# Kernel tuning notes

Measured on AMD Instinct MI355X. Metric: run time of the kernel, lower is better.

The kernel has to match this reference:

```python
import jax, jax.numpy as jnp
import numpy as np

DIM = 192
WH, WW = 8, 8
N = WH * WW           # 64 tokens per window
H = 6                 # heads
HD = DIM // H         # 32
SCALE = HD ** -0.5
B_ = 8192             # num_windows * batch
NW = 64               # windows sharing one mask


def _relative_position_index():
    ch, cw = np.arange(WH), np.arange(WW)
    coords = np.stack(np.meshgrid(ch, cw, indexing='ij'))        # (2, Wh, Ww)
    cf = coords.reshape(2, -1)                                   # (2, N)
    rel = cf[:, :, None] - cf[:, None, :]                        # (2, N, N)
    rel = rel.transpose(1, 2, 0).copy()
    rel[:, :, 0] += WH - 1
    rel[:, :, 1] += WW - 1
    rel[:, :, 0] *= 2 * WW - 1
    return (rel.sum(-1)).astype(np.int32)                        # (N, N)


def setup_inputs() -> dict:
    key = jax.random.key(0)
    ks = jax.random.split(key, 6)
    x = jax.random.normal(ks[0], (B_, N, DIM), dtype=jnp.float32)
    mask = jnp.zeros((NW, N, N), dtype=jnp.float32)
    qkv_w = jax.random.normal(ks[1], (3 * DIM, DIM), dtype=jnp.float32) * 0.02
    qkv_b = jnp.zeros((3 * DIM,), dtype=jnp.float32)
    proj_w = jax.random.normal(ks[2], (DIM, DIM), dtype=jnp.float32) * 0.02
    proj_b = jnp.zeros((DIM,), dtype=jnp.float32)
    bias_table = jax.random.normal(ks[3], ((2 * WH - 1) * (2 * WW - 1), H), dtype=jnp.float32) * 0.02
    rel_idx = jnp.asarray(_relative_position_index())
    return {"x": x, "mask": mask, "qkv_w": qkv_w, "qkv_b": qkv_b,
            "proj_w": proj_w, "proj_b": proj_b, "bias_table": bias_table,
            "rel_idx": rel_idx}


def reference(x, mask, qkv_w, qkv_b, proj_w, proj_b, bias_table, rel_idx):
    b, n, c = x.shape
    # qkv projection -> (3, B_, H, N, HD)
    qkv = (x @ qkv_w.T + qkv_b).reshape(b, n, 3, H, HD).transpose(2, 0, 3, 1, 4)
    q, k, v = qkv[0], qkv[1], qkv[2]
    # gathered relative position bias: (H, N, N)
    rpb = bias_table[rel_idx.reshape(-1)].reshape(n, n, H).transpose(2, 0, 1)
    # attention scores with bias + per-window shift mask
    scores = jnp.einsum('bhnd,bhmd->bhnm', q * SCALE, k) + rpb[None]
    nw = mask.shape[0]
    scores = scores.reshape(b // nw, nw, H, n, n) + mask[None, :, None]
    scores = scores.reshape(b, H, n, n)
    attn = jax.nn.softmax(scores, axis=-1)
    out = jnp.einsum('bhnm,bhmd->bhnd', attn, v)          # (B_, H, N, HD)
    out = out.transpose(0, 2, 1, 3).reshape(b, n, c)       # b n (h d)
    return out @ proj_w.T + proj_b
```

## Files before the change

### kernel.cpp

```cpp
#include <hip/hip_runtime.h>
#include <hip/hip_bf16.h>

typedef __bf16 v8bf __attribute__((ext_vector_type(8)));
typedef float  v4f  __attribute__((ext_vector_type(4)));

#define MFMA(a,b,c) __builtin_amdgcn_mfma_f32_16x16x32_bf16((a),(b),(c),0,0,0)

__device__ __forceinline__ float loadf(const void* p, int i, int isb) {
  return isb ? (float)(((const __bf16*)p)[i]) : ((const float*)p)[i];
}

__global__ void detect_kernel(const void* __restrict__ x, int* __restrict__ flag) {
  __shared__ int cnt;
  if (threadIdx.x == 0) cnt = 0;
  __syncthreads();
  unsigned char b = ((const unsigned char*)x)[1 + 4 * (int)threadIdx.x];
  int e = b & 0x7f;
  if (e >= 0x3B && e <= 0x41) atomicAdd(&cnt, 1);
  __syncthreads();
  if (threadIdx.x == 0) *flag = (cnt >= 64) ? 1 : 0;
}

__global__ void prep_kernel(const void* __restrict__ qkv_w, const void* __restrict__ proj_w,
                            const void* __restrict__ bias_table, const int* __restrict__ rel_idx,
                            const void* __restrict__ mask, const int* __restrict__ flag,
                            __bf16* __restrict__ qkv_wf, __bf16* __restrict__ projf,
                            float* __restrict__ cmb) {
  const int isb = *flag;
  int e = blockIdx.x * 256 + threadIdx.x;
  if (e < 110592) {
    int j = e & 7, lx = (e >> 3) & 63, ks = (e >> 9) % 6, nt = e / 3072;
    int n = nt * 16 + (lx & 15), k = ks * 32 + (lx >> 4) * 8 + j;
    qkv_wf[e] = (__bf16)loadf(qkv_w, n * 192 + k, isb);
  } else if (e < 147456) {
    int e2 = e - 110592;
    int j = e2 & 7, lx = (e2 >> 3) & 63, ks = (e2 >> 9) % 6, nt = e2 / 3072;
    int n = nt * 16 + (lx & 15), k = ks * 32 + (lx >> 4) * 8 + j;
    projf[e2] = (__bf16)loadf(proj_w, n * 192 + k, isb);
  } else if (e < 147456 + 1572864) {
    int e2 = e - 147456;
    int j = e2 & 63, i = (e2 >> 6) & 63, hh = (e2 >> 12) % 6, w = e2 / 24576;
    cmb[e2] = loadf(bias_table, rel_idx[i * 64 + j] * 6 + hh, isb)
            + loadf(mask, (w * 64 + i) * 64 + j, isb);
  }
}

__global__ __launch_bounds__(384, 3)
void wattn_kernel(const void* __restrict__ x, const int* __restrict__ flag,
                  const __bf16* __restrict__ qkv_wf, const __bf16* __restrict__ projf,
                  const float* __restrict__ cmb,
                  const void* __restrict__ qkv_b, const void* __restrict__ proj_b,
                  void* __restrict__ out) {
  __shared__ char smem[73728];
  __bf16* xf = (__bf16*)smem;
  __bf16* Qr = (__bf16*)(smem + 24576);

  const int isb = *flag;
  const int win = blockIdx.x;
  const int t = threadIdx.x;
  const int l = t & 63;
  const int h = t >> 6;
  const int quad = l >> 4;
  const int c16 = l & 15;
  const float SCALE = 0.17677669529663687f;

  #pragma unroll
  for (int i = 0; i < 4; ++i) {
    int c = t + i * 384;
    int tok = c / 24, kb8 = c % 24;
    v8bf v;
    if (isb) {
      v = *(const v8bf*)((const __bf16*)x + (size_t)win * 12288 + (size_t)c * 8);
    } else {
      const float* xp = (const float*)x + (size_t)win * 12288 + (size_t)c * 8;
      float4 f0 = ((const float4*)xp)[0];
      float4 f1 = ((const float4*)xp)[1];
      v8bf tv;
      tv[0]=(__bf16)f0.x; tv[1]=(__bf16)f0.y; tv[2]=(__bf16)f0.z; tv[3]=(__bf16)f0.w;
      tv[4]=(__bf16)f1.x; tv[5]=(__bf16)f1.y; tv[6]=(__bf16)f1.z; tv[7]=(__bf16)f1.w;
      v = tv;
    }
    int mt = tok >> 4, r = tok & 15, ks = kb8 >> 2, kb = kb8 & 3;
    *(v8bf*)(xf + ((mt * 6 + ks) * 64 + kb * 16 + r) * 8) = v;
  }
  __syncthreads();

  const v4f vzero = {0.f, 0.f, 0.f, 0.f};

  v4f acc[4][4];
  #pragma unroll
  for (int n = 0; n < 4; ++n)
    #pragma unroll
    for (int m = 0; m < 4; ++m) acc[n][m] = vzero;

  #pragma unroll
  for (int ks = 0; ks < 6; ++ks) {
    v8bf a[4];
    #pragma unroll
    for (int mt = 0; mt < 4; ++mt) a[mt] = *(const v8bf*)(xf + ((mt * 6 + ks) * 64 + l) * 8);
    #pragma unroll
    for (int ntl = 0; ntl < 4; ++ntl) {
      int nt = (ntl < 2) ? (2 * h + ntl) : (12 + 2 * h + (ntl - 2));
      v8bf b = *(const v8bf*)(qkv_wf + ((nt * 6 + ks) * 64 + l) * 8);
      #pragma unroll
      for (int mt = 0; mt < 4; ++mt) acc[ntl][mt] = MFMA(a[mt], b, acc[ntl][mt]);
    }
  }

  __bf16* qf = Qr + h * 4096;
  __bf16* kf = qf + 2048;
  #pragma unroll
  for (int ntl = 0; ntl < 4; ++ntl) {
    int hd = (ntl & 1) * 16 + c16;
    int nglob = ((ntl < 2) ? 0 : 192) + h * 32 + hd;
    float bias = loadf(qkv_b, nglob, isb);
    float mul = (ntl < 2) ? SCALE : 1.0f;
    __bf16* dst = (ntl < 2) ? qf : kf;
    #pragma unroll
    for (int mt = 0; mt < 4; ++mt)
      #pragma unroll
      for (int reg = 0; reg < 4; ++reg) {
        float vv = (acc[ntl][mt][reg] + bias) * mul;
        int u = mt * 64 + (hd >> 3) * 16 + quad * 4 + reg;
        dst[u * 8 + (hd & 7)] = (__bf16)vv;
      }
  }

  {
    v8bf aq[4];
    #pragma unroll
    for (int mt = 0; mt < 4; ++mt) aq[mt] = *(const v8bf*)(qf + (mt * 64 + l) * 8);
    #pragma unroll
    for (int n = 0; n < 4; ++n)
      #pragma unroll
      for (int m = 0; m < 4; ++m) acc[m][n] = vzero;
    #pragma unroll
    for (int j = 0; j < 4; ++j) {
      v8bf bk = *(const v8bf*)(kf + (j * 64 + l) * 8);
      #pragma unroll
      for (int mt = 0; mt < 4; ++mt) acc[mt][j] = MFMA(aq[mt], bk, acc[mt][j]);
    }
  }
  __bf16* Pf = Qr + h * 4096;
  {
    const float* cb = cmb + (size_t)((win & 63) * 6 + h) * 4096;
    #pragma unroll
    for (int mt = 0; mt < 4; ++mt)
      #pragma unroll
      for (int reg = 0; reg < 4; ++reg) {
        int mrow = quad * 4 + reg;
        int row = mt * 16 + mrow;
        float v0 = acc[mt][0][reg] + cb[row * 64 + c16];
        float v1 = acc[mt][1][reg] + cb[row * 64 + 16 + c16];
        float v2 = acc[mt][2][reg] + cb[row * 64 + 32 + c16];
        float v3 = acc[mt][3][reg] + cb[row * 64 + 48 + c16];
        float mx = fmaxf(fmaxf(v0, v1), fmaxf(v2, v3));
        mx = fmaxf(mx, __shfl_xor(mx, 1));
        mx = fmaxf(mx, __shfl_xor(mx, 2));
        mx = fmaxf(mx, __shfl_xor(mx, 4));
        mx = fmaxf(mx, __shfl_xor(mx, 8));
        float p0 = __expf(v0 - mx), p1 = __expf(v1 - mx);
        float p2 = __expf(v2 - mx), p3 = __expf(v3 - mx);
        float sm = p0 + p1 + p2 + p3;
        sm += __shfl_xor(sm, 1);
        sm += __shfl_xor(sm, 2);
        sm += __shfl_xor(sm, 4);
        sm += __shfl_xor(sm, 8);
        float inv = 1.0f / sm;
        float pn[4] = {p0 * inv, p1 * inv, p2 * inv, p3 * inv};
        #pragma unroll
        for (int j = 0; j < 4; ++j) {
          int u = (mt * 2 + (j >> 1)) * 64 + ((j & 1) * 2 + (c16 >> 3)) * 16 + mrow;
          Pf[u * 8 + (c16 & 7)] = (__bf16)pn[j];
        }
      }
  }

  v4f vac[2][4];
  #pragma unroll
  for (int n = 0; n < 2; ++n)
    #pragma unroll
    for (int m = 0; m < 4; ++m) vac[n][m] = vzero;
  #pragma unroll
  for (int ks = 0; ks < 6; ++ks) {
    v8bf a[4];
    #pragma unroll
    for (int mt = 0; mt < 4; ++mt) a[mt] = *(const v8bf*)(xf + ((mt * 6 + ks) * 64 + l) * 8);
    #pragma unroll
    for (int ntl = 0; ntl < 2; ++ntl) {
      int nt = 24 + 2 * h + ntl;
      v8bf b = *(const v8bf*)(qkv_wf + ((nt * 6 + ks) * 64 + l) * 8);
      #pragma unroll
      for (int mt = 0; mt < 4; ++mt) vac[ntl][mt] = MFMA(a[mt], b, vac[ntl][mt]);
    }
  }
  __syncthreads();

  __bf16* vf = xf + h * 2048;
  #pragma unroll
  for (int ntl = 0; ntl < 2; ++ntl) {
    float bias = loadf(qkv_b, 384 + h * 32 + ntl * 16 + c16, isb);
    #pragma unroll
    for (int mt = 0; mt < 4; ++mt)
      #pragma unroll
      for (int reg = 0; reg < 4; ++reg) {
        int mrow = quad * 4 + reg;
        int u = (ntl * 2 + (mt >> 1)) * 64 + ((mt & 1) * 2 + (mrow >> 3)) * 16 + c16;
        vf[u * 8 + (mrow & 7)] = (__bf16)(vac[ntl][mt][reg] + bias);
      }
  }

  v4f o[4][2];
  #pragma unroll
  for (int m = 0; m < 4; ++m) { o[m][0] = vzero; o[m][1] = vzero; }
  #pragma unroll
  for (int ksb = 0; ksb < 2; ++ksb) {
    v8bf ap[4], bv[2];
    #pragma unroll
    for (int mt = 0; mt < 4; ++mt) ap[mt] = *(const v8bf*)(Pf + ((mt * 2 + ksb) * 64 + l) * 8);
    #pragma unroll
    for (int ntb = 0; ntb < 2; ++ntb) bv[ntb] = *(const v8bf*)(vf + ((ntb * 2 + ksb) * 64 + l) * 8);
    #pragma unroll
    for (int mt = 0; mt < 4; ++mt)
      #pragma unroll
      for (int ntb = 0; ntb < 2; ++ntb) o[mt][ntb] = MFMA(ap[mt], bv[ntb], o[mt][ntb]);
  }
  __syncthreads();

  __bf16* Of = Qr;
  #pragma unroll
  for (int mt = 0; mt < 4; ++mt)
    #pragma unroll
    for (int ntb = 0; ntb < 2; ++ntb)
      #pragma unroll
      for (int reg = 0; reg < 4; ++reg) {
        int u = (mt * 6 + h) * 64 + (ntb * 2 + (c16 >> 3)) * 16 + quad * 4 + reg;
        Of[u * 8 + (c16 & 7)] = (__bf16)o[mt][ntb][reg];
      }
  __syncthreads();

  v4f pa[2][4];
  #pragma unroll
  for (int n = 0; n < 2; ++n)
    #pragma unroll
    for (int m = 0; m < 4; ++m) pa[n][m] = vzero;
  #pragma unroll
  for (int ks = 0; ks < 6; ++ks) {
    v8bf a[4];
    #pragma unroll
    for (int mt = 0; mt < 4; ++mt) a[mt] = *(const v8bf*)(Of + ((mt * 6 + ks) * 64 + l) * 8);
    #pragma unroll
    for (int ntl = 0; ntl < 2; ++ntl) {
      int nt = 2 * h + ntl;
      v8bf b = *(const v8bf*)(projf + ((nt * 6 + ks) * 64 + l) * 8);
      #pragma unroll
      for (int mt = 0; mt < 4; ++mt) pa[ntl][mt] = MFMA(a[mt], b, pa[ntl][mt]);
    }
  }
  #pragma unroll
  for (int ntl = 0; ntl < 2; ++ntl) {
    int col = (2 * h + ntl) * 16 + c16;
    float pb = loadf(proj_b, col, isb);
    #pragma unroll
    for (int mt = 0; mt < 4; ++mt)
      #pragma unroll
      for (int reg = 0; reg < 4; ++reg) {
        float vv = pa[ntl][mt][reg] + pb;
        size_t oi = (size_t)win * 12288 + (size_t)(mt * 16 + quad * 4 + reg) * 192 + col;
        if (isb) ((__bf16*)out)[oi] = (__bf16)vv;
        else     ((float*)out)[oi] = vv;
      }
  }
}

extern "C" void kernel_launch(void* const* d_in, const int* in_sizes, int n_in,
                              void* d_out, int out_size, void* d_ws, size_t ws_size,
                              hipStream_t stream) {
  (void)in_sizes; (void)n_in; (void)out_size; (void)ws_size;
  const void* x          = d_in[0];
  const void* mask       = d_in[1];
  const void* qkv_w      = d_in[2];
  const void* qkv_b      = d_in[3];
  const void* proj_w     = d_in[4];
  const void* proj_b     = d_in[5];
  const void* bias_table = d_in[6];
  const int*  rel_idx    = (const int*)d_in[7];

  char* ws = (char*)d_ws;
  int*    flag    = (int*)ws;
  __bf16* qkv_wf  = (__bf16*)(ws + 256);
  __bf16* projf   = (__bf16*)(ws + 256 + 221184);
  float*  cmb     = (float*)(ws + 295168);

  detect_kernel<<<1, 256, 0, stream>>>(x, flag);
  prep_kernel<<<6720, 256, 0, stream>>>(qkv_w, proj_w, bias_table, rel_idx, mask, flag,
                                        qkv_wf, projf, cmb);
  wattn_kernel<<<8192, 384, 0, stream>>>(x, flag, qkv_wf, projf, cmb, qkv_b, proj_b, d_out);
}
```

Measured before the change: 1.074 ms.

## Cut register pressure for 4 blocks/CU and vectorize combined-bias loads

```diff
diff --git a/kernel.cpp b/kernel.cpp
--- a/kernel.cpp
+++ b/kernel.cpp
@@ -40,12 +40,13 @@
   } else if (e < 147456 + 1572864) {
     int e2 = e - 147456;
     int j = e2 & 63, i = (e2 >> 6) & 63, hh = (e2 >> 12) % 6, w = e2 / 24576;
-    cmb[e2] = loadf(bias_table, rel_idx[i * 64 + j] * 6 + hh, isb)
+    float v = loadf(bias_table, rel_idx[i * 64 + j] * 6 + hh, isb)
             + loadf(mask, (w * 64 + i) * 64 + j, isb);
-  }
-}
-
-__global__ __launch_bounds__(384, 3)
+    cmb[(e2 & ~63) | (((j & 15) << 2) | (j >> 4))] = v;
+  }
+}
+
+__global__ __launch_bounds__(384, 4)
 void wattn_kernel(const void* __restrict__ x, const int* __restrict__ flag,
                   const __bf16* __restrict__ qkv_wf, const __bf16* __restrict__ projf,
                   const float* __restrict__ cmb,
@@ -86,74 +87,69 @@
   __syncthreads();
 
   const v4f vzero = {0.f, 0.f, 0.f, 0.f};
-
-  v4f acc[4][4];
-  #pragma unroll
-  for (int n = 0; n < 4; ++n)
-    #pragma unroll
-    for (int m = 0; m < 4; ++m) acc[n][m] = vzero;
-
-  #pragma unroll
-  for (int ks = 0; ks < 6; ++ks) {
-    v8bf a[4];
-    #pragma unroll
-    for (int mt = 0; mt < 4; ++mt) a[mt] = *(const v8bf*)(xf + ((mt * 6 + ks) * 64 + l) * 8);
-    #pragma unroll
-    for (int ntl = 0; ntl < 4; ++ntl) {
-      int nt = (ntl < 2) ? (2 * h + ntl) : (12 + 2 * h + (ntl - 2));
-      v8bf b = *(const v8bf*)(qkv_wf + ((nt * 6 + ks) * 64 + l) * 8);
-      #pragma unroll
-      for (int mt = 0; mt < 4; ++mt) acc[ntl][mt] = MFMA(a[mt], b, acc[ntl][mt]);
-    }
-  }
-
   __bf16* qf = Qr + h * 4096;
   __bf16* kf = qf + 2048;
-  #pragma unroll
-  for (int ntl = 0; ntl < 4; ++ntl) {
-    int hd = (ntl & 1) * 16 + c16;
-    int nglob = ((ntl < 2) ? 0 : 192) + h * 32 + hd;
-    float bias = loadf(qkv_b, nglob, isb);
-    float mul = (ntl < 2) ? SCALE : 1.0f;
-    __bf16* dst = (ntl < 2) ? qf : kf;
-    #pragma unroll
-    for (int mt = 0; mt < 4; ++mt)
-      #pragma unroll
-      for (int reg = 0; reg < 4; ++reg) {
-        float vv = (acc[ntl][mt][reg] + bias) * mul;
-        int u = mt * 64 + (hd >> 3) * 16 + quad * 4 + reg;
-        dst[u * 8 + (hd & 7)] = (__bf16)vv;
-      }
-  }
-
+
+  #pragma unroll
+  for (int pass = 0; pass < 2; ++pass) {
+    v4f acc[2][4];
+    #pragma unroll
+    for (int n = 0; n < 2; ++n)
+      #pragma unroll
+      for (int m = 0; m < 4; ++m) acc[n][m] = vzero;
+
+    #pragma unroll
+    for (int ks = 0; ks < 6; ++ks) {
+      v8bf a[4];
+      #pragma unroll
+      for (int mt = 0; mt < 4; ++mt) a[mt] = *(const v8bf*)(xf + ((mt * 6 + ks) * 64 + l) * 8);
+      #pragma unroll
+      for (int nl = 0; nl < 2; ++nl) {
+        int nt = pass * 12 + 2 * h + nl;
+        v8bf b = *(const v8bf*)(qkv_wf + ((nt * 6 + ks) * 64 + l) * 8);
+        #pragma unroll
+        for (int mt = 0; mt < 4; ++mt) acc[nl][mt] = MFMA(a[mt], b, acc[nl][mt]);
+      }
+    }
+    __bf16* dst = pass ? kf : qf;
+    float mul = pass ? 1.0f : SCALE;
+    #pragma unroll
+    for (int nl = 0; nl < 2; ++nl) {
+      int hd = nl * 16 + c16;
+      float bias = loadf(qkv_b, pass * 192 + h * 32 + hd, isb);
+      #pragma unroll
+      for (int mt = 0; mt < 4; ++mt)
+        #pragma unroll
+        for (int reg = 0; reg < 4; ++reg) {
+          float vv = (acc[nl][mt][reg] + bias) * mul;
+          int u = mt * 64 + (hd >> 3) * 16 + quad * 4 + reg;
+          dst[u * 8 + (hd & 7)] = (__bf16)vv;
+        }
+    }
+  }
+
+  __bf16* Pf = qf;
   {
-    v8bf aq[4];
+    v8bf aq[4], bk[4];
     #pragma unroll
     for (int mt = 0; mt < 4; ++mt) aq[mt] = *(const v8bf*)(qf + (mt * 64 + l) * 8);
     #pragma unroll
-    for (int n = 0; n < 4; ++n)
-      #pragma unroll
-      for (int m = 0; m < 4; ++m) acc[m][n] = vzero;
-    #pragma unroll
-    for (int j = 0; j < 4; ++j) {
-      v8bf bk = *(const v8bf*)(kf + (j * 64 + l) * 8);
-      #pragma unroll
-      for (int mt = 0; mt < 4; ++mt) acc[mt][j] = MFMA(aq[mt], bk, acc[mt][j]);
-    }
-  }
-  __bf16* Pf = Qr + h * 4096;
-  {
+    for (int j = 0; j < 4; ++j) bk[j] = *(const v8bf*)(kf + (j * 64 + l) * 8);
     const float* cb = cmb + (size_t)((win & 63) * 6 + h) * 4096;
     #pragma unroll
-    for (int mt = 0; mt < 4; ++mt)
+    for (int mt = 0; mt < 4; ++mt) {
+      v4f sc[4];
+      #pragma unroll
+      for (int j = 0; j < 4; ++j) sc[j] = MFMA(aq[mt], bk[j], vzero);
       #pragma unroll
       for (int reg = 0; reg < 4; ++reg) {
         int mrow = quad * 4 + reg;
         int row = mt * 16 + mrow;
-        float v0 = acc[mt][0][reg] + cb[row * 64 + c16];
-        float v1 = acc[mt][1][reg] + cb[row * 64 + 16 + c16];
-        float v2 = acc[mt][2][reg] + cb[row * 64 + 32 + c16];
-        float v3 = acc[mt][3][reg] + cb[row * 64 + 48 + c16];
+        float4 cv = *(const float4*)(cb + row * 64 + c16 * 4);
+        float v0 = sc[0][reg] + cv.x;
+        float v1 = sc[1][reg] + cv.y;
+        float v2 = sc[2][reg] + cv.z;
+        float v3 = sc[3][reg] + cv.w;
         float mx = fmaxf(fmaxf(v0, v1), fmaxf(v2, v3));
         mx = fmaxf(mx, __shfl_xor(mx, 1));
         mx = fmaxf(mx, __shfl_xor(mx, 2));
@@ -174,6 +170,7 @@
           Pf[u * 8 + (c16 & 7)] = (__bf16)pn[j];
         }
       }
+    }
   }
 
   v4f vac[2][4];
```

After: 1.046 ms. 1.03x faster.
